# Kernel tuning notes

Hardware: AMD Instinct MI355X
Metric: run time of the kernel (lower is better)

Reference implementation:

```python
import jax, jax.numpy as jnp
import numpy as np

B, IN_CH, OUT_CH = 4, 5, 2
NLAT, NLON = 121, 240
LMAX = 47
L = LMAX + 1            # number of l (and m) modes kept
EMBED = 256
LAYERS = 4


def _legendre_table():
    """Orthonormalized associated Legendre functions P[l, m, lat] on an
    equiangular latitude grid, plus midpoint quadrature weights."""
    theta = np.pi * (np.arange(NLAT) + 0.5) / NLAT
    x = np.cos(theta)
    s = np.sin(theta)
    P = np.zeros((L, L, NLAT), dtype=np.float64)
    P[0, 0] = 1.0 / np.sqrt(4.0 * np.pi)
    for m in range(1, L):
        P[m, m] = np.sqrt((2.0 * m + 1.0) / (2.0 * m)) * s * P[m - 1, m - 1]
    for m in range(L - 1):
        P[m + 1, m] = np.sqrt(2.0 * m + 3.0) * x * P[m, m]
    for m in range(L):
        for l in range(m + 2, L):
            a = np.sqrt((4.0 * l * l - 1.0) / (l * l - m * m))
            b = np.sqrt(((l - 1.0) ** 2 - m * m) / (4.0 * (l - 1.0) ** 2 - 1.0))
            P[l, m] = a * (x * P[l - 1, m] - b * P[l - 2, m])
    w = (np.pi / NLAT) * s  # sin(theta) quadrature weights
    return P.astype(np.float32), w.astype(np.float32)


def setup_inputs() -> dict:
    key = jax.random.key(0)
    ks = jax.random.split(key, 10)
    P, w = _legendre_table()
    H2 = 2 * EMBED
    return {
        "x": jax.random.normal(ks[0], (B, IN_CH, NLAT, NLON), jnp.float32),
        "eps": jax.random.normal(ks[1], (B, OUT_CH, NLAT, NLON), jnp.float32),
        "Pmat": jnp.asarray(P),                 # [L, M, nlat]
        "wq": jnp.asarray(w),                   # [nlat]
        "w_in": jax.random.normal(ks[2], (EMBED, IN_CH), jnp.float32) / np.sqrt(IN_CH),
        "b_in": jnp.zeros((EMBED,), jnp.float32),
        "filt_r": jax.random.normal(ks[3], (LAYERS, EMBED, EMBED, L), jnp.float32) / np.sqrt(EMBED),
        "filt_i": jax.random.normal(ks[4], (LAYERS, EMBED, EMBED, L), jnp.float32) / np.sqrt(EMBED),
        "w1": jax.random.normal(ks[5], (LAYERS, EMBED, H2), jnp.float32) / np.sqrt(EMBED),
        "b1": jnp.zeros((LAYERS, H2), jnp.float32),
        "w2": jax.random.normal(ks[6], (LAYERS, H2, EMBED), jnp.float32) / np.sqrt(H2),
        "b2": jnp.zeros((LAYERS, EMBED), jnp.float32),
        "w_out": jax.random.normal(ks[7], (2 * OUT_CH, EMBED), jnp.float32) / np.sqrt(EMBED),
        "b_out": jnp.zeros((2 * OUT_CH,), jnp.float32),
    }


def reference(x, eps, Pmat, wq, w_in, b_in, filt_r, filt_i, w1, b1, w2, b2, w_out, b_out):
    PW = Pmat * wq  # fold quadrature weights into analysis matrix [L, M, nlat]
    # proj_in: 1x1 conv == per-pixel linear
    h = jnp.einsum('bchw,oc->bohw', x, w_in) + b_in[None, :, None, None]
    for i in range(LAYERS):
        # real SHT: longitudinal rFFT then Legendre analysis
        G = 2.0 * jnp.pi * jnp.fft.rfft(h, axis=-1, norm='forward')[..., :L]  # [b,c,lat,m]
        coeffs = jnp.einsum('bcjm,lmj->bclm', G, PW)                          # [b,c,l,m] complex
        # complex spectral filter (per-l channel mixing)
        filt = filt_r[i] + 1j * filt_i[i]
        coeffs = jnp.einsum('bilm,iol->bolm', coeffs, filt)
        # inverse SHT: Legendre synthesis then irFFT
        c = jnp.einsum('bolm,lmj->bojm', coeffs, Pmat)
        x_hat = jnp.fft.irfft(c, n=NLON, axis=-1, norm='forward')             # [b,c,lat,lon] real
        # pooled MLP residual (dropout in eval mode -> identity)
        g = jnp.mean(x_hat, axis=(-1, -2))                                    # [b,c]
        delta = jax.nn.gelu(g @ w1[i] + b1[i], approximate=False) @ w2[i] + b2[i]
        h = h + delta[:, :, None, None]
    out = jnp.einsum('bchw,oc->bohw', h, w_out) + b_out[None, :, None, None]
    mu, log_sigma = out[:, :OUT_CH], out[:, OUT_CH:]
    sample = mu + eps * jnp.exp(log_sigma)
    return (sample, mu, log_sigma)
```

## Files before the change

kernel.cpp:

```cpp
#include <hip/hip_runtime.h>
#include <hip/hip_bf16.h>


namespace {

constexpr float kTwoPi = 6.283185307179586f;
constexpr int NOUT_ITEMS = 4 * 121 * 60;

typedef float f32x4 __attribute__((ext_vector_type(4)));

constexpr int WS_PW0  = 16;
constexpr int WS_PBAR = 5824;
constexpr int WS_TW   = 5872;
constexpr int WS_XBAR = 5920;
constexpr int WS_BAR  = 8352;
constexpr int WS_G    = 10496;
constexpr int WS_BIAS = 14592;
constexpr int WS_T    = 16384;
constexpr int WS_PART = 147456;
constexpr int WS_DP   = 409600;
constexpr int WS_W1B  = 475136;
constexpr int WS_W2B  = 737280;
constexpr int WS_YP   = 1000448;

#define GF(lay, b, oq) ((((lay) * 4 + (b)) * 4 + (oq)) * 16)
#define DF(lay, hs) (1024 + ((lay) * 16 + (hs)) * 16)
#define BF(b) (2048 + (b) * 16)
constexpr int NFLAGS = 2112;

struct Args {
  const void *x, *eps, *Pmat, *wq, *w_in, *b_in, *filt_r;
  const void *w1, *b1, *w2, *b2, *w_out, *b_out;
  float* ws;
  void* out;
};

__device__ __forceinline__ float bf2f(unsigned short u) {
  union { unsigned int i; float f; } v; v.i = (unsigned int)u << 16; return v.f;
}
__device__ __forceinline__ unsigned short f2bf(float f) {
  union { float f; unsigned int i; } v; v.f = f;
  return (unsigned short)((v.i + 0x7FFFu + ((v.i >> 16) & 1u)) >> 16);
}
__device__ __forceinline__ int detect_bf(const void* wq) {
  float v = ((const float*)wq)[0];
  return !(v > 2.5e-4f && v < 4.5e-4f);
}
__device__ __forceinline__ float ldf(const void* p, long i, int bf) {
  return bf ? bf2f(((const unsigned short*)p)[i]) : ((const float*)p)[i];
}
__device__ __forceinline__ float4 ld4(const void* p, long e, int bf) {
  if (bf) {
    ushort4 u = *(const ushort4*)((const unsigned short*)p + e);
    return make_float4(bf2f(u.x), bf2f(u.y), bf2f(u.z), bf2f(u.w));
  }
  return *(const float4*)((const float*)p + e);
}
__device__ __forceinline__ void st4(void* p, long e, float a, float b, float c,
                                    float d, int bf) {
  if (bf) {
    ushort4 u; u.x = f2bf(a); u.y = f2bf(b); u.z = f2bf(c); u.w = f2bf(d);
    *(ushort4*)((unsigned short*)p + e) = u;
  } else {
    *(float4*)((float*)p + e) = make_float4(a, b, c, d);
  }
}

__device__ __forceinline__ void stw4(float* p, f32x4 v) {
  asm volatile("global_store_dwordx4 %0, %1, off sc0 sc1"
               :: "v"(p), "v"(v) : "memory");
}
__device__ __forceinline__ void stg_agent_i(int* p, int v) {
  __hip_atomic_store(p, v, __ATOMIC_RELAXED, __HIP_MEMORY_SCOPE_AGENT);
}
__device__ __forceinline__ int ldg_agent_i(const int* p) {
  return __hip_atomic_load(p, __ATOMIC_RELAXED, __HIP_MEMORY_SCOPE_AGENT);
}

__global__ void k01_prep_xbar(Args A) {
  int bf = detect_bf(A.wq);
  float* ws = A.ws;
  int t = threadIdx.x;
  int bx = blockIdx.x;
  if (bx >= 606) {
    int cv = bx - 606;
    const void* src = (cv < 32) ? A.w1 : A.w2;
    unsigned short* dst = (unsigned short*)(ws + ((cv < 32) ? WS_W1B : WS_W2B));
    long base = (long)(cv & 31) * 16384;
#pragma unroll 4
    for (int k = 0; k < 16; ++k) {
      long e = base + ((long)k * 256 + t) * 4;
      float4 v = ld4(src, e, bf);
      ushort4 o;
      o.x = f2bf(v.x); o.y = f2bf(v.y); o.z = f2bf(v.z); o.w = f2bf(v.w);
      *(ushort4*)(dst + e) = o;
    }
    return;
  }
  if (bx == 605) {
    __shared__ float praw[48 * 121];
    __shared__ float pwv[48 * 121];
    for (int i = t; i < NFLAGS; i += 256) ((int*)(ws + WS_BAR))[i] = 0;
    for (int idx = t; idx < 48 * 121; idx += 256) {
      int l = idx / 121, j = idx - l * 121;
      float p = ldf(A.Pmat, (long)l * 48 * 121 + j, bf);
      float w = ldf(A.wq, j, bf);
      praw[idx] = p;
      pwv[idx] = p * w;
      ws[WS_PW0 + idx] = p * w;
    }
    __syncthreads();
    if (t < 48) {
      float pb = 0.f, sw = 0.f;
      const float* pr = &praw[t * 121];
      const float* pw = &pwv[t * 121];
      for (int j = 0; j < 121; ++j) { pb += pr[j]; sw += pw[j]; }
      pb *= (1.0f / 121.0f);
      ws[WS_PBAR + t] = pb;
      ws[WS_TW + t] = kTwoPi * pb * sw;
    }
    return;
  }
  int wave = bx * 4 + (t >> 6);
  int lane = t & 63;
  long base = (long)wave * 240;
  float s = 0.f;
  for (int e = lane; e < 240; e += 64) s += ldf(A.x, base + e, bf);
  for (int d = 32; d; d >>= 1) s += __shfl_xor(s, d, 64);
  if (lane == 0) ws[WS_XBAR + wave] = s * (1.0f / 240.0f);
}

__global__ void __launch_bounds__(256) kY(Args A) {
  __shared__ float pw0[48 * 121];
  __shared__ float xb[605];
  int b = blockIdx.x;
  int t = threadIdx.x;
  float* ws = A.ws;
  for (int i = t; i < 48 * 121; i += 256) pw0[i] = ws[WS_PW0 + i];
  for (int i = t; i < 605; i += 256) xb[i] = ws[WS_XBAR + b * 605 + i];
  __syncthreads();
  if (t < 240) {
    int ic = t / 48, l = t - ic * 48;
    float s = 0.f;
    const float* pw = &pw0[l * 121];
    const float* xx = &xb[ic * 121];
    for (int j = 0; j < 121; ++j) s += pw[j] * xx[j];
    ws[WS_YP + (b * 5 + ic) * 48 + l] = kTwoPi * ws[WS_PBAR + l] * s;
  }
}

__global__ void __launch_bounds__(256) k3(Args A) {
  __shared__ float qs[4][4][48];
  __shared__ float ypl[960];
  __shared__ float twl[48];
  int bf = detect_bf(A.wq);
  int t = threadIdx.x;
  int bx = blockIdx.x;
  float* ws = A.ws;
  int lay = bx >> 8;
  int rem = bx & 255;
  int cb = rem >> 2, ob = rem & 3;
  int c0 = cb * 4, o0 = ob * 64;
  int ol = t >> 2, lq = t & 3;
  if (t < 48) twl[t] = ws[WS_TW + t];
  for (int i = t; i < 960; i += 256) ypl[i] = ws[WS_YP + i];
  __syncthreads();
  for (int dd = t; dd < 768; dd += 256) {
    int bb = dd / 192, r2 = dd - bb * 192;
    int ci = r2 / 48, l = r2 - ci * 48;
    int c = c0 + ci;
    float s = ldf(A.b_in, c, bf) * twl[l];
#pragma unroll
    for (int ic = 0; ic < 5; ++ic)
      s += ldf(A.w_in, c * 5 + ic, bf) * ypl[(bb * 5 + ic) * 48 + l];
    qs[bb][ci][l] = s;
  }
  __syncthreads();

  float acc0 = 0.f, acc1 = 0.f, acc2 = 0.f, acc3 = 0.f;
#pragma unroll
  for (int ci = 0; ci < 4; ++ci) {
    int c = c0 + ci;
    long base = ((long)((lay * 256 + c) * 256 + (o0 + ol))) * 48 + lq * 12;
    float f[12];
    if (bf) {
      const uint2* up = (const uint2*)((const unsigned short*)A.filt_r + base);
      uint2 u0 = up[0], u1 = up[1], u2 = up[2];
      f[0] = bf2f((unsigned short)(u0.x & 0xFFFFu)); f[1] = bf2f((unsigned short)(u0.x >> 16));
      f[2] = bf2f((unsigned short)(u0.y & 0xFFFFu)); f[3] = bf2f((unsigned short)(u0.y >> 16));
      f[4] = bf2f((unsigned short)(u1.x & 0xFFFFu)); f[5] = bf2f((unsigned short)(u1.x >> 16));
      f[6] = bf2f((unsigned short)(u1.y & 0xFFFFu)); f[7] = bf2f((unsigned short)(u1.y >> 16));
      f[8] = bf2f((unsigned short)(u2.x & 0xFFFFu)); f[9] = bf2f((unsigned short)(u2.x >> 16));
      f[10] = bf2f((unsigned short)(u2.y & 0xFFFFu)); f[11] = bf2f((unsigned short)(u2.y >> 16));
    } else {
      const float4* fp = (const float4*)((const float*)A.filt_r + base);
      float4 v0 = fp[0], v1 = fp[1], v2 = fp[2];
      f[0] = v0.x; f[1] = v0.y; f[2] = v0.z; f[3] = v0.w;
      f[4] = v1.x; f[5] = v1.y; f[6] = v1.z; f[7] = v1.w;
      f[8] = v2.x; f[9] = v2.y; f[10] = v2.z; f[11] = v2.w;
    }
    float tacc = 0.f;
    int lb = lq * 12;
#pragma unroll
    for (int r = 0; r < 12; ++r) {
      float fv = f[r];
      int l = lb + r;
      tacc += fv * twl[l];
      acc0 += fv * qs[0][ci][l];
      acc1 += fv * qs[1][ci][l];
      acc2 += fv * qs[2][ci][l];
      acc3 += fv * qs[3][ci][l];
    }
    tacc += __shfl_xor(tacc, 1, 64);
    tacc += __shfl_xor(tacc, 2, 64);
    if (lq == 0)
      ((unsigned short*)(ws + WS_T))[((lay * 256 + c) * 256) + o0 + ol] =
          f2bf(tacc);
  }
  acc0 += __shfl_xor(acc0, 1, 64); acc0 += __shfl_xor(acc0, 2, 64);
  acc1 += __shfl_xor(acc1, 1, 64); acc1 += __shfl_xor(acc1, 2, 64);
  acc2 += __shfl_xor(acc2, 1, 64); acc2 += __shfl_xor(acc2, 2, 64);
  acc3 += __shfl_xor(acc3, 1, 64); acc3 += __shfl_xor(acc3, 2, 64);
  if (lq == 0) {
    int po = o0 + ol;
    long pb = (long)(lay * 64 + cb) * 4 * 256;
    ws[WS_PART + pb + 0 * 256 + po] = acc0;
    ws[WS_PART + pb + 1 * 256 + po] = acc1;
    ws[WS_PART + pb + 2 * 256 + po] = acc2;
    ws[WS_PART + pb + 3 * 256 + po] = acc3;
  }
}

__device__ __forceinline__ void load_item(const Args& A, int idx, int bf,
                                          float4 xv[5], float4 ev[2]) {
  int n4 = idx % 60;
  int j = (idx / 60) % 121;
  int bb = idx / 7260;
  int n = n4 * 4;
#pragma unroll
  for (int ic = 0; ic < 5; ++ic)
    xv[ic] = ld4(A.x, ((long)((bb * 5 + ic) * 121 + j)) * 240 + n, bf);
#pragma unroll
  for (int oc = 0; oc < 2; ++oc)
    ev[oc] = ld4(A.eps, ((long)((bb * 2 + oc) * 121 + j)) * 240 + n, bf);
}

__device__ __forceinline__ void store_item(const Args& A, int idx, int bf,
                                           const float4 xv[5], const float4 ev[2],
                                           const float* sW4, const float* sBias) {
  int n4 = idx % 60;
  int j = (idx / 60) % 121;
  int bb = idx / 7260;
  int n = n4 * 4;
  float v[4][4];
#pragma unroll
  for (int o4 = 0; o4 < 4; ++o4) {
    float bias = sBias[bb * 4 + o4];
    float s0 = bias, s1 = bias, s2 = bias, s3 = bias;
#pragma unroll
    for (int ic = 0; ic < 5; ++ic) {
      float w = sW4[o4 * 5 + ic];
      s0 += w * xv[ic].x; s1 += w * xv[ic].y;
      s2 += w * xv[ic].z; s3 += w * xv[ic].w;
    }
    v[o4][0] = s0; v[o4][1] = s1; v[o4][2] = s2; v[o4][3] = s3;
  }
  const long NPO = (long)4 * 2 * 121 * 240;
#pragma unroll
  for (int oc = 0; oc < 2; ++oc) {
    long eoff = ((long)((bb * 2 + oc) * 121 + j)) * 240 + n;
    float e0 = expf(v[oc + 2][0]), e1 = expf(v[oc + 2][1]);
    float e2 = expf(v[oc + 2][2]), e3 = expf(v[oc + 2][3]);
    st4(A.out, eoff, v[oc][0] + ev[oc].x * e0, v[oc][1] + ev[oc].y * e1,
        v[oc][2] + ev[oc].z * e2, v[oc][3] + ev[oc].w * e3, bf);
    st4(A.out, NPO + eoff, v[oc][0], v[oc][1], v[oc][2], v[oc][3], bf);
    st4(A.out, 2 * NPO + eoff, v[oc + 2][0], v[oc + 2][1], v[oc + 2][2],
        v[oc + 2][3], bf);
  }
}

__global__ void __launch_bounds__(1024, 1) kchain(Args A) {
  __shared__ __align__(16) char sm[49152];
  int bf = detect_bf(A.wq);
  int t = threadIdx.x;
  int blk = blockIdx.x;
  float* ws = A.ws;
  int* bars = (int*)(ws + WS_BAR);

  if (blk < 64) {
    unsigned short* sT = (unsigned short*)sm;
    float* sR = (float*)(sm + 32768);
    float* sDr = (float*)(sm + 36864);
    float* sD = (float*)(sm + 40960);
    float* sGo = (float*)(sm + 41984);
    int lay = blk >> 4, b = (blk >> 2) & 3, oq = blk & 3;
    int o = t & 63, grp = t >> 6;
    if (lay) {
      const uint4* Tsrc = (const uint4*)((const unsigned short*)(ws + WS_T));
      uint4* sT4 = (uint4*)sT;
      for (int i = t; i < 2048; i += 1024) {
        int c = i >> 3, k = i & 7;
        sT4[i] = Tsrc[(lay * 256 + c) * 32 + oq * 8 + k];
      }
    }
    {
      float acc = 0.f;
#pragma unroll
      for (int i = 0; i < 4; ++i)
        acc += ws[WS_PART + (((lay * 64 + grp * 4 + i) * 4 + b) * 256) +
                  oq * 64 + o];
      sR[grp * 64 + o] = acc;
    }
    if (lay) {
      if (t < 16) {
        while (ldg_agent_i(&bars[DF(lay - 1, t)]) == 0)
          __builtin_amdgcn_s_sleep(2);
      }
      __syncthreads();
      {
        int c = t & 255, g4 = t >> 8;
        float d = 0.f;
        for (int l = 0; l < lay; ++l)
#pragma unroll
          for (int k = 0; k < 4; ++k)
            d += ws[WS_DP + (((l * 16 + g4 * 4 + k) * 4 + b) * 256) + c];
        sDr[g4 * 256 + c] = d;
      }
      __syncthreads();
      if (t < 256)
        sD[t] = sDr[t] + sDr[256 + t] + sDr[512 + t] + sDr[768 + t];
      __syncthreads();
      float p = 0.f;
#pragma unroll
      for (int k = 0; k < 16; ++k) {
        int c2 = grp * 16 + k;
        p += sD[c2] * bf2f(sT[c2 * 64 + o]);
      }
      sR[grp * 64 + o] += p;
    }
    __syncthreads();
    if (t < 64) {
      float g = 0.f;
#pragma unroll
      for (int i = 0; i < 16; ++i) g += sR[i * 64 + t];
      sGo[t] = g;
    }
    __syncthreads();
    if (t < 16)
      stw4(ws + WS_G + ((lay * 4 + b) * 256) + oq * 64 + t * 4,
           *(const f32x4*)&sGo[t * 4]);
    asm volatile("s_waitcnt vmcnt(0)" ::: "memory");
    __syncthreads();
    if (t == 0) stg_agent_i(&bars[GF(lay, b, oq)], 1);
    return;
  }

  if (blk < 128) {
    unsigned short* w1s = (unsigned short*)sm;
    unsigned short* w2s = (unsigned short*)(sm + 16384);
    float* sg = (float*)(sm + 32768);
    float* sAp = (float*)(sm + 36864);
    float* sA = (float*)(sm + 40960);
    float* sDp = (float*)(sm + 41984);
    int m = blk - 64;
    int lay = m >> 4, hs = m & 15;
    {
      const uint4* W1s4 = (const uint4*)(ws + WS_W1B);
      int o = t >> 2, k = t & 3;
      ((uint4*)w1s)[t] = W1s4[(lay * 256 + o) * 64 + hs * 4 + k];
      const uint4* W2s4 = (const uint4*)(ws + WS_W2B);
      int hl = t >> 5, k2 = t & 31;
      ((uint4*)w2s)[t] = W2s4[(lay * 512 + hs * 32 + hl) * 32 + k2];
    }
    if (t < 16) {
      while (ldg_agent_i(&bars[GF(lay, t >> 2, t & 3)]) == 0)
        __builtin_amdgcn_s_sleep(2);
    }
    __syncthreads();
    if (t < 256) {
      int bb = t >> 6, o4 = (t & 63) * 4;
      *(f32x4*)&sg[bb * 256 + o4] =
          *(const f32x4*)(ws + WS_G + ((lay * 4 + bb) * 256) + o4);
    }
    __syncthreads();
    {
      int bb = t >> 8, hl = (t >> 3) & 31, ocs = t & 7;
      float p = 0.f;
#pragma unroll
      for (int j = 0; j < 32; ++j) {
        int o = ocs * 32 + j;
        p += sg[bb * 256 + o] * bf2f(w1s[o * 32 + hl]);
      }
      sAp[(bb * 32 + hl) * 8 + ocs] = p;
    }
    __syncthreads();
    if (t < 128) {
      int bb = t >> 5, hl = t & 31;
      float v = ldf(A.b1, lay * 512 + hs * 32 + hl, bf);
#pragma unroll
      for (int k = 0; k < 8; ++k) v += sAp[(bb * 32 + hl) * 8 + k];
      sA[bb * 32 + hl] = 0.5f * v * (1.0f + erff(v * 0.7071067811865475f));
    }
    __syncthreads();
    {
      int bb = t >> 8, c = t & 255;
      float d = (hs == 0) ? ldf(A.b2, lay * 256 + c, bf) : 0.f;
#pragma unroll
      for (int hl = 0; hl < 32; ++hl)
        d += sA[bb * 32 + hl] * bf2f(w2s[hl * 256 + c]);
      sDp[bb * 256 + c] = d;
    }
    __syncthreads();
    if (t < 256) {
      int bb = t >> 6, c4 = (t & 63) * 4;
      stw4(ws + WS_DP + (((lay * 16 + hs) * 4 + bb) * 256) + c4,
           *(const f32x4*)&sDp[bb * 256 + c4]);
    }
    asm volatile("s_waitcnt vmcnt(0)" ::: "memory");
    __syncthreads();
    if (t == 0) stg_agent_i(&bars[DF(lay, hs)], 1);
    return;
  }

  if (blk < 132) {
    float* sDr16 = (float*)sm;
    float* sD = (float*)(sm + 16384);
    float* sBs = (float*)(sm + 17408);
    int b = blk - 128;
    if (t < 16) {
      while (ldg_agent_i(&bars[DF(3, t)]) == 0) __builtin_amdgcn_s_sleep(2);
    }
    __syncthreads();
    {
      int grp = t >> 6, c4 = (t & 63) * 4;
      f32x4 d = {0.f, 0.f, 0.f, 0.f};
#pragma unroll
      for (int k = 0; k < 4; ++k) {
        int idx = grp * 4 + k;
        d += *(const f32x4*)(ws + WS_DP +
                             ((((idx >> 4) * 16 + (idx & 15)) * 4 + b) * 256) +
                             c4);
      }
      *(f32x4*)&sDr16[grp * 256 + c4] = d;
    }
    __syncthreads();
    if (t < 256) {
      float d = 0.f;
#pragma unroll
      for (int g = 0; g < 16; ++g) d += sDr16[g * 256 + t];
      sD[t] = d;
    }
    __syncthreads();
    if (t < 256) {
      int o4 = t >> 6, sub = t & 63;
      float s = 0.f;
      for (int c = sub; c < 256; c += 64)
        s += ldf(A.w_out, o4 * 256 + c, bf) * (ldf(A.b_in, c, bf) + sD[c]);
      for (int dd = 32; dd; dd >>= 1) s += __shfl_xor(s, dd, 64);
      if (sub == 0) sBs[o4] = ldf(A.b_out, o4, bf) + s;
    }
    __syncthreads();
    if (t == 0) stw4(ws + WS_BIAS + b * 4, *(const f32x4*)&sBs[0]);
    asm volatile("s_waitcnt vmcnt(0)" ::: "memory");
    __syncthreads();
    if (t == 0) stg_agent_i(&bars[BF(b)], 1);
    return;
  }

  {
    float* sW4 = (float*)sm;
    float* sBias = (float*)(sm + 128);
    int gid = (blk - 132) * 1024 + t;
    bool has = gid < NOUT_ITEMS;
    float4 xv[5], ev[2];
    if (has) load_item(A, gid, bf, xv, ev);
    if (t < 160) {
      int e = t >> 3, sub8 = t & 7;
      int o4b = e / 5, ic = e - o4b * 5;
      float w = 0.f;
      for (int c = sub8; c < 256; c += 8)
        w += ldf(A.w_out, o4b * 256 + c, bf) * ldf(A.w_in, c * 5 + ic, bf);
      w += __shfl_xor(w, 1, 64);
      w += __shfl_xor(w, 2, 64);
      w += __shfl_xor(w, 4, 64);
      if (sub8 == 0) sW4[e] = w;
    }
    if (t < 4) {
      while (ldg_agent_i(&bars[BF(t)]) == 0) __builtin_amdgcn_s_sleep(8);
    }
    __syncthreads();
    if (t < 16) sBias[t] = ws[WS_BIAS + t];
    __syncthreads();
    if (has) store_item(A, gid, bf, xv, ev, sW4, sBias);
  }
}

}

extern "C" void kernel_launch(void* const* d_in, const int* in_sizes, int n_in,
                              void* d_out, int out_size, void* d_ws,
                              size_t ws_size, hipStream_t stream) {
  Args A;
  A.x = d_in[0]; A.eps = d_in[1]; A.Pmat = d_in[2]; A.wq = d_in[3];
  A.w_in = d_in[4]; A.b_in = d_in[5]; A.filt_r = d_in[6];
  A.w1 = d_in[8]; A.b1 = d_in[9]; A.w2 = d_in[10]; A.b2 = d_in[11];
  A.w_out = d_in[12]; A.b_out = d_in[13];
  A.ws = (float*)d_ws;
  A.out = d_out;

  hipLaunchKernelGGL(k01_prep_xbar, dim3(670), dim3(256), 0, stream, A);
  hipLaunchKernelGGL(kY, dim3(4), dim3(256), 0, stream, A);
  hipLaunchKernelGGL(k3, dim3(1024), dim3(256), 0, stream, A);
  hipLaunchKernelGGL(kchain, dim3(164), dim3(1024), 0, stream, A);
}
```

Baseline: 80.67 us.

## Precompose T with W1 in a new kernel to shorten the serial layer chain

Adds a kernel kU that precomputes U = T·W1 per layer, plus the static first-layer pre-activation (pooled partials times W1 plus b1), outside the barrier-chained kernel. The chain then merges the former g-blocks and MLP blocks into one stage per layer, removing one inter-block flag wait per layer. The output stage now uses 256 active threads per block over more blocks, and the spin-sleep intervals are shortened. The cost is one extra launch, an extra bf16 rounding of U, and more global traffic to build U.

```diff
diff --git a/kernel.cpp b/kernel.cpp
--- a/kernel.cpp
+++ b/kernel.cpp
@@ -14,7 +14,6 @@
 constexpr int WS_TW   = 5872;
 constexpr int WS_XBAR = 5920;
 constexpr int WS_BAR  = 8352;
-constexpr int WS_G    = 10496;
 constexpr int WS_BIAS = 14592;
 constexpr int WS_T    = 16384;
 constexpr int WS_PART = 147456;
@@ -22,10 +21,11 @@
 constexpr int WS_W1B  = 475136;
 constexpr int WS_W2B  = 737280;
 constexpr int WS_YP   = 1000448;
-
-#define GF(lay, b, oq) ((((lay) * 4 + (b)) * 4 + (oq)) * 16)
-#define DF(lay, hs) (1024 + ((lay) * 16 + (hs)) * 16)
-#define BF(b) (2048 + (b) * 16)
+constexpr int WS_U    = 1001472;
+constexpr int WS_AB   = 1263616;
+
+#define DF(lay, hs) (((lay) * 16 + (hs)) * 16)
+#define BF(b) (1024 + (b) * 16)
 constexpr int NFLAGS = 2112;
 
 struct Args {
@@ -231,6 +231,73 @@
   }
 }
 
+__global__ void __launch_bounds__(1024) kU(Args A) {
+  int t = threadIdx.x;
+  int bx = blockIdx.x;
+  float* ws = A.ws;
+  const unsigned short* W1u = (const unsigned short*)(ws + WS_W1B);
+
+  if (bx < 128) {
+    __shared__ float tls[8 * 256];
+    int lay = bx >> 5, cs = bx & 31;
+    int c0 = cs * 8;
+    const unsigned short* Tu = (const unsigned short*)(ws + WS_T);
+    for (int i = t; i < 2048; i += 1024) {
+      int cc = i >> 8, o = i & 255;
+      tls[cc * 256 + o] = bf2f(Tu[(lay * 256 + c0 + cc) * 256 + o]);
+    }
+    __syncthreads();
+    int h = t & 511, cg = t >> 9;
+    float acc[4] = {0.f, 0.f, 0.f, 0.f};
+    const unsigned short* w1p = W1u + (long)(lay * 256) * 512 + h;
+#pragma unroll 4
+    for (int o = 0; o < 256; ++o) {
+      float wv = bf2f(w1p[(long)o * 512]);
+#pragma unroll
+      for (int k = 0; k < 4; ++k)
+        acc[k] += tls[(cg * 4 + k) * 256 + o] * wv;
+    }
+    unsigned short* Uu = (unsigned short*)(ws + WS_U);
+#pragma unroll
+    for (int k = 0; k < 4; ++k)
+      Uu[(long)(lay * 256 + c0 + cg * 4 + k) * 512 + h] = f2bf(acc[k]);
+    return;
+  }
+
+  {
+    __shared__ float sP[4][256];
+    __shared__ float gb[256];
+    __shared__ float sH[2][512];
+    int ab = bx - 128;
+    int lay = ab >> 2, b = ab & 3;
+    int bf = detect_bf(A.wq);
+    {
+      int q = t >> 8, o = t & 255;
+      float s = 0.f;
+#pragma unroll
+      for (int i = 0; i < 16; ++i)
+        s += ws[WS_PART + (((lay * 64 + q * 16 + i) * 4 + b) * 256) + o];
+      sP[q][o] = s;
+    }
+    __syncthreads();
+    if (t < 256) gb[t] = sP[0][t] + sP[1][t] + sP[2][t] + sP[3][t];
+    __syncthreads();
+    {
+      int h = t & 511, half = t >> 9;
+      float s = 0.f;
+      const unsigned short* w1p = W1u + (long)(lay * 256) * 512 + h;
+#pragma unroll 4
+      for (int o = half * 128; o < half * 128 + 128; ++o)
+        s += gb[o] * bf2f(w1p[(long)o * 512]);
+      sH[half][h] = s;
+    }
+    __syncthreads();
+    if (t < 512)
+      ws[WS_AB + (lay * 4 + b) * 512 + t] =
+          ldf(A.b1, lay * 512 + t, bf) + sH[0][t] + sH[1][t];
+  }
+}
+
 __device__ __forceinline__ void load_item(const Args& A, int idx, int bf,
                                           float4 xv[5], float4 ev[2]) {
   int n4 = idx % 60;
@@ -288,133 +355,84 @@
   int* bars = (int*)(ws + WS_BAR);
 
   if (blk < 64) {
-    unsigned short* sT = (unsigned short*)sm;
-    float* sR = (float*)(sm + 32768);
-    float* sDr = (float*)(sm + 36864);
-    float* sD = (float*)(sm + 40960);
-    float* sGo = (float*)(sm + 41984);
-    int lay = blk >> 4, b = (blk >> 2) & 3, oq = blk & 3;
-    int o = t & 63, grp = t >> 6;
+    unsigned short* Us = (unsigned short*)sm;
+    unsigned short* w2s = (unsigned short*)(sm + 16384);
+    float* dynf = (float*)(sm + 32768);
+    int lay = blk >> 4, hs = blk & 15;
+    const unsigned short* Uu = (const unsigned short*)(ws + WS_U);
+    const unsigned short* W2u = (const unsigned short*)(ws + WS_W2B);
     if (lay) {
-      const uint4* Tsrc = (const uint4*)((const unsigned short*)(ws + WS_T));
-      uint4* sT4 = (uint4*)sT;
       for (int i = t; i < 2048; i += 1024) {
         int c = i >> 3, k = i & 7;
-        sT4[i] = Tsrc[(lay * 256 + c) * 32 + oq * 8 + k];
-      }
-    }
-    {
-      float acc = 0.f;
-#pragma unroll
-      for (int i = 0; i < 4; ++i)
-        acc += ws[WS_PART + (((lay * 64 + grp * 4 + i) * 4 + b) * 256) +
-                  oq * 64 + o];
-      sR[grp * 64 + o] = acc;
+        ((ushort4*)Us)[i] =
+            *(const ushort4*)(Uu + (long)(lay * 256 + c) * 512 + hs * 32 + k * 4);
+      }
+    }
+    for (int i = t; i < 2048; i += 1024) {
+      int hl = i >> 6, k = i & 63;
+      ((ushort4*)w2s)[i] =
+          *(const ushort4*)(W2u + (long)(lay * 512 + hs * 32 + hl) * 256 + k * 4);
     }
     if (lay) {
       if (t < 16) {
         while (ldg_agent_i(&bars[DF(lay - 1, t)]) == 0)
-          __builtin_amdgcn_s_sleep(2);
+          __builtin_amdgcn_s_sleep(1);
       }
       __syncthreads();
       {
-        int c = t & 255, g4 = t >> 8;
-        float d = 0.f;
+        int b = t >> 8, sq = (t >> 6) & 3, c4 = (t & 63) * 4;
+        f32x4 d = {0.f, 0.f, 0.f, 0.f};
         for (int l = 0; l < lay; ++l)
 #pragma unroll
           for (int k = 0; k < 4; ++k)
-            d += ws[WS_DP + (((l * 16 + g4 * 4 + k) * 4 + b) * 256) + c];
-        sDr[g4 * 256 + c] = d;
+            d += *(const f32x4*)(ws + WS_DP +
+                                 (((l * 16 + sq * 4 + k) * 4 + b) * 256) + c4);
+        *(f32x4*)&dynf[sq * 1024 + b * 256 + c4] = d;
       }
       __syncthreads();
-      if (t < 256)
-        sD[t] = sDr[t] + sDr[256 + t] + sDr[512 + t] + sDr[768 + t];
+      {
+        float v = dynf[t] + dynf[1024 + t] + dynf[2048 + t] + dynf[3072 + t];
+        __syncthreads();
+        dynf[t] = v;
+      }
       __syncthreads();
-      float p = 0.f;
-#pragma unroll
-      for (int k = 0; k < 16; ++k) {
-        int c2 = grp * 16 + k;
-        p += sD[c2] * bf2f(sT[c2 * 64 + o]);
-      }
-      sR[grp * 64 + o] += p;
-    }
-    __syncthreads();
-    if (t < 64) {
-      float g = 0.f;
-#pragma unroll
-      for (int i = 0; i < 16; ++i) g += sR[i * 64 + t];
-      sGo[t] = g;
-    }
-    __syncthreads();
-    if (t < 16)
-      stw4(ws + WS_G + ((lay * 4 + b) * 256) + oq * 64 + t * 4,
-           *(const f32x4*)&sGo[t * 4]);
-    asm volatile("s_waitcnt vmcnt(0)" ::: "memory");
-    __syncthreads();
-    if (t == 0) stg_agent_i(&bars[GF(lay, b, oq)], 1);
-    return;
-  }
-
-  if (blk < 128) {
-    unsigned short* w1s = (unsigned short*)sm;
-    unsigned short* w2s = (unsigned short*)(sm + 16384);
-    float* sg = (float*)(sm + 32768);
-    float* sAp = (float*)(sm + 36864);
-    float* sA = (float*)(sm + 40960);
-    float* sDp = (float*)(sm + 41984);
-    int m = blk - 64;
-    int lay = m >> 4, hs = m & 15;
+      {
+        int b = t >> 8, hl = (t >> 3) & 31, cs = t & 7;
+        float p = 0.f;
+#pragma unroll
+        for (int j = 0; j < 32; ++j) {
+          int c = cs * 32 + j;
+          p += dynf[b * 256 + c] * bf2f(Us[c * 32 + hl]);
+        }
+        dynf[1024 + b * 256 + hl * 8 + cs] = p;
+      }
+      __syncthreads();
+    } else {
+      __syncthreads();
+    }
+    if (t < 128) {
+      int b = t >> 5, hl = t & 31;
+      float v = ws[WS_AB + (lay * 4 + b) * 512 + hs * 32 + hl];
+      if (lay) {
+#pragma unroll
+        for (int k = 0; k < 8; ++k) v += dynf[1024 + b * 256 + hl * 8 + k];
+      }
+      dynf[2048 + b * 32 + hl] = 0.5f * v * (1.0f + erff(v * 0.7071067811865475f));
+    }
+    __syncthreads();
     {
-      const uint4* W1s4 = (const uint4*)(ws + WS_W1B);
-      int o = t >> 2, k = t & 3;
-      ((uint4*)w1s)[t] = W1s4[(lay * 256 + o) * 64 + hs * 4 + k];
-      const uint4* W2s4 = (const uint4*)(ws + WS_W2B);
-      int hl = t >> 5, k2 = t & 31;
-      ((uint4*)w2s)[t] = W2s4[(lay * 512 + hs * 32 + hl) * 32 + k2];
-    }
-    if (t < 16) {
-      while (ldg_agent_i(&bars[GF(lay, t >> 2, t & 3)]) == 0)
-        __builtin_amdgcn_s_sleep(2);
+      int b = t >> 8, c = t & 255;
+      float d = (hs == 0) ? ldf(A.b2, lay * 256 + c, bf) : 0.f;
+#pragma unroll
+      for (int hl = 0; hl < 32; ++hl)
+        d += dynf[2048 + b * 32 + hl] * bf2f(w2s[hl * 256 + c]);
+      dynf[2304 + b * 256 + c] = d;
     }
     __syncthreads();
     if (t < 256) {
-      int bb = t >> 6, o4 = (t & 63) * 4;
-      *(f32x4*)&sg[bb * 256 + o4] =
-          *(const f32x4*)(ws + WS_G + ((lay * 4 + bb) * 256) + o4);
-    }
-    __syncthreads();
-    {
-      int bb = t >> 8, hl = (t >> 3) & 31, ocs = t & 7;
-      float p = 0.f;
-#pragma unroll
-      for (int j = 0; j < 32; ++j) {
-        int o = ocs * 32 + j;
-        p += sg[bb * 256 + o] * bf2f(w1s[o * 32 + hl]);
-      }
-      sAp[(bb * 32 + hl) * 8 + ocs] = p;
-    }
-    __syncthreads();
-    if (t < 128) {
-      int bb = t >> 5, hl = t & 31;
-      float v = ldf(A.b1, lay * 512 + hs * 32 + hl, bf);
-#pragma unroll
-      for (int k = 0; k < 8; ++k) v += sAp[(bb * 32 + hl) * 8 + k];
-      sA[bb * 32 + hl] = 0.5f * v * (1.0f + erff(v * 0.7071067811865475f));
-    }
-    __syncthreads();
-    {
-      int bb = t >> 8, c = t & 255;
-      float d = (hs == 0) ? ldf(A.b2, lay * 256 + c, bf) : 0.f;
-#pragma unroll
-      for (int hl = 0; hl < 32; ++hl)
-        d += sA[bb * 32 + hl] * bf2f(w2s[hl * 256 + c]);
-      sDp[bb * 256 + c] = d;
-    }
-    __syncthreads();
-    if (t < 256) {
-      int bb = t >> 6, c4 = (t & 63) * 4;
-      stw4(ws + WS_DP + (((lay * 16 + hs) * 4 + bb) * 256) + c4,
-           *(const f32x4*)&sDp[bb * 256 + c4]);
+      int b = t >> 6, c4 = (t & 63) * 4;
+      stw4(ws + WS_DP + (((lay * 16 + hs) * 4 + b) * 256) + c4,
+           *(const f32x4*)&dynf[2304 + b * 256 + c4]);
     }
     asm volatile("s_waitcnt vmcnt(0)" ::: "memory");
     __syncthreads();
@@ -422,26 +440,24 @@
     return;
   }
 
-  if (blk < 132) {
+  if (blk < 68) {
     float* sDr16 = (float*)sm;
     float* sD = (float*)(sm + 16384);
     float* sBs = (float*)(sm + 17408);
-    int b = blk - 128;
+    int b = blk - 64;
     if (t < 16) {
-      while (ldg_agent_i(&bars[DF(3, t)]) == 0) __builtin_amdgcn_s_sleep(2);
+      while (ldg_agent_i(&bars[DF(3, t)]) == 0) __builtin_amdgcn_s_sleep(1);
     }
     __syncthreads();
     {
-      int grp = t >> 6, c4 = (t & 63) * 4;
+      int sq = t >> 6, c4 = (t & 63) * 4;
       f32x4 d = {0.f, 0.f, 0.f, 0.f};
 #pragma unroll
       for (int k = 0; k < 4; ++k) {
-        int idx = grp * 4 + k;
-        d += *(const f32x4*)(ws + WS_DP +
-                             ((((idx >> 4) * 16 + (idx & 15)) * 4 + b) * 256) +
-                             c4);
-      }
-      *(f32x4*)&sDr16[grp * 256 + c4] = d;
+        int idx = sq * 4 + k;
+        d += *(const f32x4*)(ws + WS_DP + ((idx * 4 + b) * 256) + c4);
+      }
+      *(f32x4*)&sDr16[sq * 256 + c4] = d;
     }
     __syncthreads();
     if (t < 256) {
@@ -470,10 +486,18 @@
   {
     float* sW4 = (float*)sm;
     float* sBias = (float*)(sm + 128);
-    int gid = (blk - 132) * 1024 + t;
-    bool has = gid < NOUT_ITEMS;
+    int gid = (blk - 68) * 256 + t;
+    bool has = (t < 256) && (gid < NOUT_ITEMS);
     float4 xv[5], ev[2];
-    if (has) load_item(A, gid, bf, xv, ev);
+    if (has) {
+      load_item(A, gid, bf, xv, ev);
+#pragma unroll
+      for (int ic = 0; ic < 5; ++ic)
+        asm volatile("" :: "v"(*(const f32x4*)&xv[ic]));
+#pragma unroll
+      for (int oc = 0; oc < 2; ++oc)
+        asm volatile("" :: "v"(*(const f32x4*)&ev[oc]));
+    }
     if (t < 160) {
       int e = t >> 3, sub8 = t & 7;
       int o4b = e / 5, ic = e - o4b * 5;
@@ -486,7 +510,7 @@
       if (sub8 == 0) sW4[e] = w;
     }
     if (t < 4) {
-      while (ldg_agent_i(&bars[BF(t)]) == 0) __builtin_amdgcn_s_sleep(8);
+      while (ldg_agent_i(&bars[BF(t)]) == 0) __builtin_amdgcn_s_sleep(4);
     }
     __syncthreads();
     if (t < 16) sBias[t] = ws[WS_BIAS + t];
@@ -511,5 +535,6 @@
   hipLaunchKernelGGL(k01_prep_xbar, dim3(670), dim3(256), 0, stream, A);
   hipLaunchKernelGGL(kY, dim3(4), dim3(256), 0, stream, A);
   hipLaunchKernelGGL(k3, dim3(1024), dim3(256), 0, stream, A);
-  hipLaunchKernelGGL(kchain, dim3(164), dim3(1024), 0, stream, A);
-}
+  hipLaunchKernelGGL(kU, dim3(144), dim3(1024), 0, stream, A);
+  hipLaunchKernelGGL(kchain, dim3(184), dim3(1024), 0, stream, A);
+}
```

After: 92.03 us. 14.1% more time.

## Fuse xbar reduction and Legendre projection into single prep kernel

Applied to the files above, without the earlier changes.

The separate x-mean kernel and the small kY projection kernel are merged into one prep kernel. Each of 20 blocks handles one (batch, channel) pair: it loads Pmat and the quadrature weights into shared memory, reduces x over longitude with float4 loads, and projects onto the Legendre modes directly. This removes one kernel launch and the intermediate global round-trips through PW0, XBAR and PBAR. In exchange, every block recomputes the Pmat slice and its row means redundantly.

```diff
diff --git a/kernel.cpp b/kernel.cpp
--- a/kernel.cpp
+++ b/kernel.cpp
@@ -9,13 +9,10 @@
 
 typedef float f32x4 __attribute__((ext_vector_type(4)));
 
-constexpr int WS_PW0  = 16;
-constexpr int WS_PBAR = 5824;
-constexpr int WS_TW   = 5872;
-constexpr int WS_XBAR = 5920;
 constexpr int WS_BAR  = 8352;
 constexpr int WS_G    = 10496;
 constexpr int WS_BIAS = 14592;
+constexpr int WS_TW   = 15616;
 constexpr int WS_T    = 16384;
 constexpr int WS_PART = 147456;
 constexpr int WS_DP   = 409600;
@@ -77,13 +74,14 @@
   return __hip_atomic_load(p, __ATOMIC_RELAXED, __HIP_MEMORY_SCOPE_AGENT);
 }
 
-__global__ void k01_prep_xbar(Args A) {
+__global__ void __launch_bounds__(256) kprep(Args A) {
   int bf = detect_bf(A.wq);
   float* ws = A.ws;
   int t = threadIdx.x;
   int bx = blockIdx.x;
-  if (bx >= 606) {
-    int cv = bx - 606;
+
+  if (bx >= 21) {
+    int cv = bx - 21;
     const void* src = (cv < 32) ? A.w1 : A.w2;
     unsigned short* dst = (unsigned short*)(ws + ((cv < 32) ? WS_W1B : WS_W2B));
     long base = (long)(cv & 31) * 16384;
@@ -97,55 +95,60 @@
     }
     return;
   }
-  if (bx == 605) {
-    __shared__ float praw[48 * 121];
-    __shared__ float pwv[48 * 121];
+
+  __shared__ float praw[48 * 121];
+  __shared__ float wqs[121];
+  __shared__ float pbars[48];
+  for (int i = t; i < 121; i += 256) wqs[i] = ldf(A.wq, i, bf);
+  for (int i = t; i < 5808; i += 256)
+    praw[i] = ldf(A.Pmat, (long)(i / 121) * 5808 + (i % 121), bf);
+  __syncthreads();
+  if (t < 48) {
+    float pb = 0.f;
+    const float* pr = &praw[t * 121];
+    for (int j = 0; j < 121; ++j) pb += pr[j];
+    pbars[t] = pb * (1.0f / 121.0f);
+  }
+  __syncthreads();
+
+  if (bx == 20) {
     for (int i = t; i < NFLAGS; i += 256) ((int*)(ws + WS_BAR))[i] = 0;
-    for (int idx = t; idx < 48 * 121; idx += 256) {
-      int l = idx / 121, j = idx - l * 121;
-      float p = ldf(A.Pmat, (long)l * 48 * 121 + j, bf);
-      float w = ldf(A.wq, j, bf);
-      praw[idx] = p;
-      pwv[idx] = p * w;
-      ws[WS_PW0 + idx] = p * w;
-    }
-    __syncthreads();
     if (t < 48) {
-      float pb = 0.f, sw = 0.f;
+      float sw = 0.f;
       const float* pr = &praw[t * 121];
-      const float* pw = &pwv[t * 121];
-      for (int j = 0; j < 121; ++j) { pb += pr[j]; sw += pw[j]; }
-      pb *= (1.0f / 121.0f);
-      ws[WS_PBAR + t] = pb;
-      ws[WS_TW + t] = kTwoPi * pb * sw;
+      for (int j = 0; j < 121; ++j) sw += pr[j] * wqs[j];
+      ws[WS_TW + t] = kTwoPi * pbars[t] * sw;
     }
     return;
   }
-  int wave = bx * 4 + (t >> 6);
-  int lane = t & 63;
-  long base = (long)wave * 240;
-  float s = 0.f;
-  for (int e = lane; e < 240; e += 64) s += ldf(A.x, base + e, bf);
-  for (int d = 32; d; d >>= 1) s += __shfl_xor(s, d, 64);
-  if (lane == 0) ws[WS_XBAR + wave] = s * (1.0f / 240.0f);
-}
-
-__global__ void __launch_bounds__(256) kY(Args A) {
-  __shared__ float pw0[48 * 121];
-  __shared__ float xb[605];
-  int b = blockIdx.x;
-  int t = threadIdx.x;
-  float* ws = A.ws;
-  for (int i = t; i < 48 * 121; i += 256) pw0[i] = ws[WS_PW0 + i];
-  for (int i = t; i < 605; i += 256) xb[i] = ws[WS_XBAR + b * 605 + i];
+
+  __shared__ float xprt[242];
+  __shared__ float xbw[121];
+  int b = bx / 5, ic = bx - b * 5;
+  if (t < 242) {
+    int j = t >> 1, half = t & 1;
+    long base = ((long)((b * 5 + ic) * 121 + j)) * 240 + half * 120;
+    float s = 0.f;
+#pragma unroll 6
+    for (int k = 0; k < 30; ++k) {
+      float4 v = ld4(A.x, base + k * 4, bf);
+      s += v.x + v.y + v.z + v.w;
+    }
+    xprt[t] = s;
+  }
   __syncthreads();
-  if (t < 240) {
-    int ic = t / 48, l = t - ic * 48;
+  if (t < 121)
+    xbw[t] = (xprt[2 * t] + xprt[2 * t + 1]) * (1.0f / 240.0f) * wqs[t];
+  __syncthreads();
+  if (t < 96) {
+    int l = t >> 1, half = t & 1;
+    const float* pr = &praw[l * 121];
     float s = 0.f;
-    const float* pw = &pw0[l * 121];
-    const float* xx = &xb[ic * 121];
-    for (int j = 0; j < 121; ++j) s += pw[j] * xx[j];
-    ws[WS_YP + (b * 5 + ic) * 48 + l] = kTwoPi * ws[WS_PBAR + l] * s;
+    int j0 = half * 61, j1 = half ? 121 : 61;
+    for (int j = j0; j < j1; ++j) s += pr[j] * xbw[j];
+    s += __shfl_xor(s, 1, 64);
+    if (half == 0)
+      ws[WS_YP + (b * 5 + ic) * 48 + l] = kTwoPi * pbars[l] * s;
   }
 }
 
@@ -508,8 +511,7 @@
   A.ws = (float*)d_ws;
   A.out = d_out;
 
-  hipLaunchKernelGGL(k01_prep_xbar, dim3(670), dim3(256), 0, stream, A);
-  hipLaunchKernelGGL(kY, dim3(4), dim3(256), 0, stream, A);
+  hipLaunchKernelGGL(kprep, dim3(85), dim3(256), 0, stream, A);
   hipLaunchKernelGGL(k3, dim3(1024), dim3(256), 0, stream, A);
   hipLaunchKernelGGL(kchain, dim3(164), dim3(1024), 0, stream, A);
 }
```

Result: slower. 84.71 us (+5.0%).
